# Kernel optimization log

Measured on AMD Instinct MI355X. Metric: run time of the kernel, lower is better.

Reference implementation:

```python
import jax, jax.numpy as jnp
import numpy as np

EPS = 1e-5
ABIT = 8
WBIT = 8


def ste_round(x):
    # straight-through rounding (HAWQ SymmetricQuantFunction)
    return x + jax.lax.stop_gradient(jnp.round(x) - x)


def quant_act(x, bit=ABIT):
    # per-tensor symmetric activation quantization (QuantAct)
    n = 2.0 ** (bit - 1) - 1  # 127
    scale = jnp.max(jnp.abs(x)) / n
    x_int = jnp.clip(ste_round(x / scale), -n - 1, n)
    return x_int * scale, scale


def setup_inputs() -> dict:
    key = jax.random.key(0)
    k = jax.random.split(key, 6)
    B, C_in, H, W, C_out = 32, 512, 32, 32, 128
    x = jax.random.normal(k[0], (B, C_in, H, W), jnp.float32)
    # incoming activation scale (input assumed already 8-bit quantized)
    act_scaling_factor = (jnp.max(jnp.abs(x)) / 127.0).reshape(1)
    bn_gamma = jax.random.uniform(k[1], (C_in,), jnp.float32, 0.5, 1.5)
    bn_beta = jax.random.normal(k[2], (C_in,), jnp.float32) * 0.1
    bn_mean = jax.random.normal(k[3], (C_in,), jnp.float32) * 0.1
    bn_var = jax.random.uniform(k[4], (C_in,), jnp.float32, 0.5, 1.5)
    conv_weight = jax.random.normal(k[5], (C_out, C_in, 3, 3), jnp.float32) / np.sqrt(C_in * 9)
    return {"x": x, "act_scaling_factor": act_scaling_factor,
            "bn_gamma": bn_gamma, "bn_beta": bn_beta,
            "bn_mean": bn_mean, "bn_var": bn_var,
            "conv_weight": conv_weight}


def reference(x, act_scaling_factor, bn_gamma, bn_beta, bn_mean, bn_var, conv_weight):
    nw = 2.0 ** (WBIT - 1) - 1  # 127
    s_in = act_scaling_factor.reshape(())

    # ---- QuantBn: fold BN into per-channel affine, quantize weight/bias ----
    w_bn = bn_gamma / jnp.sqrt(bn_var + EPS)            # [C_in]
    b_bn = bn_beta - bn_mean * w_bn                      # [C_in]
    ws_bn = jnp.max(jnp.abs(w_bn)) / nw                  # per-tensor weight scale
    w_int = jnp.clip(ste_round(w_bn / ws_bn), -nw - 1, nw)
    bn_sf = ws_bn * s_in                                 # bn output scaling factor
    b_int = ste_round(b_bn / bn_sf)
    x_int = x / s_in
    x = (x_int * w_int[None, :, None, None] + b_int[None, :, None, None]) * bn_sf

    # ---- ReLU ----
    x = jax.nn.relu(x)

    # ---- QuantAct: requantize activations to 8 bit ----
    x, s_act = quant_act(x)

    # ---- QuantConv2d: per-output-channel 8-bit weight quant, int conv ----
    ws_c = jnp.max(jnp.abs(conv_weight), axis=(1, 2, 3)) / nw       # [C_out]
    w_cint = jnp.clip(ste_round(conv_weight / ws_c[:, None, None, None]), -nw - 1, nw)
    y_int = jax.lax.conv_general_dilated(
        x / s_act, w_cint, window_strides=(1, 1), padding=((1, 1), (1, 1)),
        dimension_numbers=("NCHW", "OIHW", "NCHW"))
    conv_sf = s_act * ws_c                               # [C_out]
    y = y_int * conv_sf[None, :, None, None]

    # ---- QuantAct output requant ----
    y, s_out = quant_act(y)
    return (y, s_out)
```

## Files before the change

kernel.cpp:

```cpp
#include <hip/hip_runtime.h>


typedef int v4i __attribute__((ext_vector_type(4)));

#define WS_A1    64
#define WS_B1    2176
#define WS_WSC   4224
#define WS_WQ    8192
#define WS_X2    602112
#define WS_ZROW  18427904

__device__ __forceinline__ float wave_max(float m) {
#pragma unroll
    for (int off = 32; off; off >>= 1) m = fmaxf(m, __shfl_xor(m, off));
    return m;
}

__global__ __launch_bounds__(512) void k_prep(
    const float* __restrict__ gamma, const float* __restrict__ beta,
    const float* __restrict__ mean,  const float* __restrict__ var,
    const float* __restrict__ asf,   const float* __restrict__ cw,
    float* ws_f, unsigned* ws_u, float* __restrict__ wsc,
    signed char* __restrict__ wq) {
    int t = threadIdx.x;
    __shared__ float red[8];
    if (blockIdx.x == 128) {
        float wbn = gamma[t] / sqrtf(var[t] + 1e-5f);
        float bbn = beta[t] - mean[t] * wbn;
        float m = wave_max(fabsf(wbn));
        if ((t & 63) == 0) red[t >> 6] = m;
        __syncthreads();
        float mall = red[0];
#pragma unroll
        for (int i = 1; i < 8; ++i) mall = fmaxf(mall, red[i]);
        float ws_bn = mall / 127.0f;
        float s_in  = asf[0];
        float bn_sf = ws_bn * s_in;
        float wint  = fminf(fmaxf(rintf(wbn / ws_bn), -128.f), 127.f);
        float bint  = rintf(bbn / bn_sf);
        ws_f[WS_A1 / 4 + t] = wint * bn_sf / s_in;
        ws_f[WS_B1 / 4 + t] = bint * bn_sf;
        if (t == 0) { ws_u[0] = 0u; ws_u[1] = 0u; }
    } else {
        int co = blockIdx.x;
        const float* w = cw + (size_t)co * 4608;
        float m = 0.f;
        for (int j = t; j < 4608; j += 512) m = fmaxf(m, fabsf(w[j]));
        m = wave_max(m);
        if ((t & 63) == 0) red[t >> 6] = m;
        __syncthreads();
        float mall = red[0];
#pragma unroll
        for (int i = 1; i < 8; ++i) mall = fmaxf(mall, red[i]);
        float sc = mall / 127.0f;
        if (t == 0) wsc[co] = sc;
        for (int j = t; j < 4608; j += 512) {
            float q = fminf(fmaxf(rintf(w[j] / sc), -128.f), 127.f);
            int c = j / 9, tap = j - c * 9;
            wq[(((size_t)tap * 8 + (c >> 6)) * 128 + co) * 64 + (c & 63)] = (signed char)q;
        }
    }
}

__global__ __launch_bounds__(256) void k_xmax(
    const float4* __restrict__ x4, const float* __restrict__ ws_f,
    unsigned* __restrict__ amax) {
    const float* A1 = ws_f + WS_A1 / 4;
    const float* B1 = ws_f + WS_B1 / 4;
    float m = 0.f;
    int stride = gridDim.x * blockDim.x;
    for (int i = blockIdx.x * blockDim.x + threadIdx.x; i < 4194304; i += stride) {
        float4 v = x4[i];
        int c = (i >> 8) & 511;
        float A = A1[c], B = B1[c];
        m = fmaxf(m, fmaxf(fmaxf(fmaf(v.x, A, B), fmaf(v.y, A, B)),
                           fmaxf(fmaf(v.z, A, B), fmaf(v.w, A, B))));
    }
    __shared__ float red[4];
    m = wave_max(m);
    if ((threadIdx.x & 63) == 0) red[threadIdx.x >> 6] = m;
    __syncthreads();
    if (threadIdx.x == 0) {
        m = fmaxf(fmaxf(red[0], red[1]), fmaxf(red[2], red[3]));
        atomicMax(amax, __float_as_uint(m));
    }
}

__global__ __launch_bounds__(256) void k_xquant(
    const float4* __restrict__ x4, const float* __restrict__ ws_f,
    const unsigned* __restrict__ amax, unsigned* __restrict__ x2u,
    unsigned* __restrict__ zrowu) {
    int bb = blockIdx.x >> 5, h = blockIdx.x & 31;
    float inv_sact = 127.0f / __uint_as_float(amax[0]);
    const float* A1 = ws_f + WS_A1 / 4;
    const float* B1 = ws_f + WS_B1 / 4;
    int t = threadIdx.x;

    {
        int cc = t >> 5, rem = t & 31;
        int wp = (rem >> 4) * 33, inner = rem & 15;
        x2u[((size_t)(((bb * 32 + h) * 8 + cc) * 34 + wp)) * 16 + inner] = 0u;
    }
    if (blockIdx.x < 17) {
        int idx = blockIdx.x * 256 + t;
        if (idx < 4352) zrowu[idx] = 0u;
    }

    __shared__ unsigned lds[512 * 9];

#pragma unroll
    for (int it = 0; it < 16; ++it) {
        int idx = it * 256 + t;
        int c = idx >> 3, f4 = idx & 7;
        float4 v = x4[((size_t)bb * 512 + c) * 256 + h * 8 + f4];
        float A = A1[c] * inv_sact, B = B1[c] * inv_sact;
        unsigned q0 = (unsigned)(int)fminf(rintf(fmaxf(fmaf(v.x, A, B), 0.f)), 127.f);
        unsigned q1 = (unsigned)(int)fminf(rintf(fmaxf(fmaf(v.y, A, B), 0.f)), 127.f);
        unsigned q2 = (unsigned)(int)fminf(rintf(fmaxf(fmaf(v.z, A, B), 0.f)), 127.f);
        unsigned q3 = (unsigned)(int)fminf(rintf(fmaxf(fmaf(v.w, A, B), 0.f)), 127.f);
        lds[c * 9 + f4] = q0 | (q1 << 8) | (q2 << 16) | (q3 << 24);
    }
    __syncthreads();

#pragma unroll
    for (int it2 = 0; it2 < 4; ++it2) {
        int cdw = (t & 31) + ((t >> 6) << 5);
        int wq4 = ((t >> 5) & 1) + (it2 << 1);
        unsigned u0 = lds[(4 * cdw + 0) * 9 + wq4];
        unsigned u1 = lds[(4 * cdw + 1) * 9 + wq4];
        unsigned u2 = lds[(4 * cdw + 2) * 9 + wq4];
        unsigned u3 = lds[(4 * cdw + 3) * 9 + wq4];
        int cc = cdw >> 4, inner = cdw & 15;
        unsigned* dst = x2u + ((size_t)(((bb * 32 + h) * 8 + cc) * 34 + wq4 * 4 + 1)) * 16 + inner;
#pragma unroll
        for (int k = 0; k < 4; ++k) {
            unsigned o = ((u0 >> (8 * k)) & 255) | (((u1 >> (8 * k)) & 255) << 8) |
                         (((u2 >> (8 * k)) & 255) << 16) | (((u3 >> (8 * k)) & 255) << 24);
            dst[(size_t)k * 16] = o;
        }
    }
}

__global__ __launch_bounds__(256, 2) void k_conv(
    const unsigned char* __restrict__ x2, const unsigned char* __restrict__ zrow,
    const signed char* __restrict__ wq,
    const float* __restrict__ wsc, const unsigned* __restrict__ amax,
    unsigned* __restrict__ amaxy, float* __restrict__ y) {
    __shared__ v4i red[2][1024];
    int t = threadIdx.x;
    int lane = t & 63, kv = t >> 6;
    int m = lane & 15, quad = lane >> 4;

    int bid = blockIdx.x;
    int tile = (bid & 7) * 128 + (bid >> 3);
    int ch = tile & 1;
    int rowpair = (tile >> 1) & 15;
    int bb = tile >> 5;
    int h0 = rowpair * 2;
    int co0 = ch * 64;

    const unsigned char* xb = x2 + (size_t)bb * (32 * 8 * 34 * 64);
    const unsigned char* rp[4];
#pragma unroll
    for (int j = 0; j < 4; ++j) {
        int row = h0 - 1 + j;
        rp[j] = ((unsigned)row < 32u) ? (xb + (size_t)row * (8 * 34 * 64)) : zrow;
    }

    v4i acc[4][4];
#pragma unroll
    for (int i = 0; i < 4; ++i)
#pragma unroll
        for (int j = 0; j < 4; ++j) acc[i][j] = (v4i){0, 0, 0, 0};

    const v4i* pwv = (const v4i*)wq + (co0 + m) * 4 + quad;

#pragma unroll
    for (int kh = 0; kh < 3; ++kh)
#pragma unroll
        for (int kw = 0; kw < 3; ++kw) {
            int tap = kh * 3 + kw;
#pragma unroll
            for (int cc = 0; cc < 2; ++cc) {
                int ci = kv * 2 + cc;
                v4i a[4];
#pragma unroll
                for (int mt = 0; mt < 4; ++mt)
                    a[mt] = *((const v4i*)rp[kh + (mt >> 1)] +
                              (ci * 34 + m + (mt & 1) * 16 + kw) * 4 + quad);
#pragma unroll
                for (int nt = 0; nt < 4; ++nt) {
                    v4i bf = pwv[tap * 4096 + ci * 512 + nt * 64];
#pragma unroll
                    for (int mt = 0; mt < 4; ++mt)
                        acc[mt][nt] = __builtin_amdgcn_mfma_i32_16x16x64_i8(a[mt], bf, acc[mt][nt], 0, 0, 0);
                }
            }
        }

    if (kv >= 2) {
#pragma unroll
        for (int mt = 0; mt < 4; ++mt)
#pragma unroll
            for (int nt = 0; nt < 4; ++nt)
                red[kv - 2][(mt * 4 + nt) * 64 + lane] = acc[mt][nt];
    }
    __syncthreads();
    if (kv < 2) {
#pragma unroll
        for (int mt = 0; mt < 4; ++mt)
#pragma unroll
            for (int nt = 0; nt < 4; ++nt) {
                v4i p = red[kv][(mt * 4 + nt) * 64 + lane];
                acc[mt][nt].x += p.x; acc[mt][nt].y += p.y;
                acc[mt][nt].z += p.z; acc[mt][nt].w += p.w;
            }
    }
    __syncthreads();
    if (kv == 1) {
#pragma unroll
        for (int mt = 0; mt < 4; ++mt)
#pragma unroll
            for (int nt = 0; nt < 4; ++nt)
                red[0][(mt * 4 + nt) * 64 + lane] = acc[mt][nt];
    }
    __syncthreads();
    if (kv == 0) {
#pragma unroll
        for (int mt = 0; mt < 4; ++mt)
#pragma unroll
            for (int nt = 0; nt < 4; ++nt) {
                v4i p = red[0][(mt * 4 + nt) * 64 + lane];
                acc[mt][nt].x += p.x; acc[mt][nt].y += p.y;
                acc[mt][nt].z += p.z; acc[mt][nt].w += p.w;
            }

        float s_act = __uint_as_float(amax[0]) / 127.0f;
        float mx = 0.f;
#pragma unroll
        for (int nt = 0; nt < 4; ++nt) {
            int co = co0 + nt * 16 + m;
            float sf = s_act * wsc[co];
#pragma unroll
            for (int mt = 0; mt < 4; ++mt) {
                int row = h0 + (mt >> 1);
                float* yb = y + ((size_t)(bb * 128 + co)) * 1024 + row * 32 + (mt & 1) * 16;
                float4 vv;
                vv.x = (float)acc[mt][nt][0] * sf;
                vv.y = (float)acc[mt][nt][1] * sf;
                vv.z = (float)acc[mt][nt][2] * sf;
                vv.w = (float)acc[mt][nt][3] * sf;
                *(float4*)(yb + quad * 4) = vv;
                mx = fmaxf(mx, fmaxf(fmaxf(fabsf(vv.x), fabsf(vv.y)),
                                     fmaxf(fabsf(vv.z), fabsf(vv.w))));
            }
        }
        mx = wave_max(mx);
        if (lane == 0) atomicMax(amaxy, __float_as_uint(mx));
    }
}

__global__ __launch_bounds__(256) void k_yquant(float* __restrict__ yout,
                                                const unsigned* __restrict__ ws_u) {
    float s_out = __uint_as_float(ws_u[1]) / 127.0f;
    float4* y4 = (float4*)yout;
    int stride = gridDim.x * blockDim.x;
    for (int i = blockIdx.x * blockDim.x + threadIdx.x; i < 1048576; i += stride) {
        float4 v = y4[i];
        v.x = fminf(fmaxf(rintf(v.x / s_out), -128.f), 127.f) * s_out;
        v.y = fminf(fmaxf(rintf(v.y / s_out), -128.f), 127.f) * s_out;
        v.z = fminf(fmaxf(rintf(v.z / s_out), -128.f), 127.f) * s_out;
        v.w = fminf(fmaxf(rintf(v.w / s_out), -128.f), 127.f) * s_out;
        y4[i] = v;
    }
    if (blockIdx.x == 0 && threadIdx.x == 0) yout[4194304] = s_out;
}

extern "C" void kernel_launch(void* const* d_in, const int* in_sizes, int n_in,
                              void* d_out, int out_size, void* d_ws, size_t ws_size,
                              hipStream_t stream) {
    const float* x     = (const float*)d_in[0];
    const float* asf   = (const float*)d_in[1];
    const float* gamma = (const float*)d_in[2];
    const float* beta  = (const float*)d_in[3];
    const float* mean  = (const float*)d_in[4];
    const float* var   = (const float*)d_in[5];
    const float* cw    = (const float*)d_in[6];

    float*    ws_f = (float*)d_ws;
    unsigned* ws_u = (unsigned*)d_ws;
    signed char*   wq   = (signed char*)d_ws + WS_WQ;
    unsigned char* x2   = (unsigned char*)d_ws + WS_X2;
    unsigned char* zrow = (unsigned char*)d_ws + WS_ZROW;
    float* y = (float*)d_out;

    k_prep<<<129, 512, 0, stream>>>(gamma, beta, mean, var, asf, cw,
                                    ws_f, ws_u, ws_f + WS_WSC / 4, wq);
    k_xmax<<<1024, 256, 0, stream>>>((const float4*)x, ws_f, ws_u);
    k_xquant<<<1024, 256, 0, stream>>>((const float4*)x, ws_f, ws_u,
                                       (unsigned*)x2, (unsigned*)zrow);
    k_conv<<<1024, 256, 0, stream>>>(x2, zrow, wq, ws_f + WS_WSC / 4,
                                     ws_u, ws_u + 1, y);
    k_yquant<<<1024, 256, 0, stream>>>(y, ws_u);
}
```

Baseline: 184.7 us.

## Derive activation max from per-channel raw min/max, drop separate xmax pass

Replaces the atomic global max over the BN-affine-transformed input with per-channel min/max of raw x computed inside the prep kernel. Because the affine map is monotonic per channel, the post-BN max can be rebuilt from those extremes, and each xquant block recomputes it redundantly. This removes the atomic and the dependency on it. The prep kernel now also reads all of x, so the extra full pass is folded into a wider launch rather than eliminated. Separately, conv occupancy is raised to 3 and the cross-wave reduction is flattened into one LDS stage, which needs a larger shared buffer.

```diff
diff --git a/kernel.cpp b/kernel.cpp
--- a/kernel.cpp
+++ b/kernel.cpp
@@ -6,7 +6,9 @@
 #define WS_A1    64
 #define WS_B1    2176
 #define WS_WSC   4224
-#define WS_WQ    8192
+#define WS_XMX   4736
+#define WS_XMN   6784
+#define WS_WQ    12288
 #define WS_X2    602112
 #define WS_ZROW  18427904
 
@@ -20,11 +22,31 @@
     const float* __restrict__ gamma, const float* __restrict__ beta,
     const float* __restrict__ mean,  const float* __restrict__ var,
     const float* __restrict__ asf,   const float* __restrict__ cw,
+    const float4* __restrict__ x4,
     float* ws_f, unsigned* ws_u, float* __restrict__ wsc,
     signed char* __restrict__ wq) {
     int t = threadIdx.x;
-    __shared__ float red[8];
-    if (blockIdx.x == 128) {
+    int bid = blockIdx.x;
+    __shared__ float red[16];
+    if (bid < 128) {
+        int co = bid;
+        const float* w = cw + (size_t)co * 4608;
+        float m = 0.f;
+        for (int j = t; j < 4608; j += 512) m = fmaxf(m, fabsf(w[j]));
+        m = wave_max(m);
+        if ((t & 63) == 0) red[t >> 6] = m;
+        __syncthreads();
+        float mall = red[0];
+#pragma unroll
+        for (int i = 1; i < 8; ++i) mall = fmaxf(mall, red[i]);
+        float sc = mall / 127.0f;
+        if (t == 0) wsc[co] = sc;
+#pragma unroll
+        for (int tap = 0; tap < 9; ++tap) {
+            float q = fminf(fmaxf(rintf(w[t * 9 + tap] / sc), -128.f), 127.f);
+            wq[(((size_t)(tap * 8 + (t >> 6)) * 128 + co) * 64) + (t & 63)] = (signed char)q;
+        }
+    } else if (bid == 128) {
         float wbn = gamma[t] / sqrtf(var[t] + 1e-5f);
         float bbn = beta[t] - mean[t] * wbn;
         float m = wave_max(fabsf(wbn));
@@ -40,61 +62,55 @@
         float bint  = rintf(bbn / bn_sf);
         ws_f[WS_A1 / 4 + t] = wint * bn_sf / s_in;
         ws_f[WS_B1 / 4 + t] = bint * bn_sf;
-        if (t == 0) { ws_u[0] = 0u; ws_u[1] = 0u; }
+        if (t == 0) ws_u[1] = 0u;
     } else {
-        int co = blockIdx.x;
-        const float* w = cw + (size_t)co * 4608;
-        float m = 0.f;
-        for (int j = t; j < 4608; j += 512) m = fmaxf(m, fabsf(w[j]));
-        m = wave_max(m);
-        if ((t & 63) == 0) red[t >> 6] = m;
+        int c = bid - 129;
+        float mx = -3.4e38f, mn = 3.4e38f;
+#pragma unroll
+        for (int r = 0; r < 16; ++r) {
+            int bbb = r * 2 + (t >> 8);
+            float4 v = x4[((size_t)(bbb * 512 + c)) * 256 + (t & 255)];
+            mx = fmaxf(mx, fmaxf(fmaxf(v.x, v.y), fmaxf(v.z, v.w)));
+            mn = fminf(mn, fminf(fminf(v.x, v.y), fminf(v.z, v.w)));
+        }
+        mx = wave_max(mx);
+        mn = -wave_max(-mn);
+        if ((t & 63) == 0) { red[t >> 6] = mx; red[8 + (t >> 6)] = mn; }
         __syncthreads();
-        float mall = red[0];
-#pragma unroll
-        for (int i = 1; i < 8; ++i) mall = fmaxf(mall, red[i]);
-        float sc = mall / 127.0f;
-        if (t == 0) wsc[co] = sc;
-        for (int j = t; j < 4608; j += 512) {
-            float q = fminf(fmaxf(rintf(w[j] / sc), -128.f), 127.f);
-            int c = j / 9, tap = j - c * 9;
-            wq[(((size_t)tap * 8 + (c >> 6)) * 128 + co) * 64 + (c & 63)] = (signed char)q;
-        }
-    }
-}
-
-__global__ __launch_bounds__(256) void k_xmax(
-    const float4* __restrict__ x4, const float* __restrict__ ws_f,
-    unsigned* __restrict__ amax) {
+        if (t == 0) {
+            float M = red[0], N = red[8];
+#pragma unroll
+            for (int i = 1; i < 8; ++i) { M = fmaxf(M, red[i]); N = fminf(N, red[8 + i]); }
+            ws_f[WS_XMX / 4 + c] = M;
+            ws_f[WS_XMN / 4 + c] = N;
+        }
+    }
+}
+
+__global__ __launch_bounds__(256) void k_xquant(
+    const float4* __restrict__ x4, float* __restrict__ ws_f,
+    unsigned* __restrict__ x2u, unsigned* __restrict__ zrowu) {
+    int bb = blockIdx.x >> 5, h = blockIdx.x & 31;
     const float* A1 = ws_f + WS_A1 / 4;
     const float* B1 = ws_f + WS_B1 / 4;
-    float m = 0.f;
-    int stride = gridDim.x * blockDim.x;
-    for (int i = blockIdx.x * blockDim.x + threadIdx.x; i < 4194304; i += stride) {
-        float4 v = x4[i];
-        int c = (i >> 8) & 511;
+    const float* XMX = ws_f + WS_XMX / 4;
+    const float* XMN = ws_f + WS_XMN / 4;
+    int t = threadIdx.x;
+
+    __shared__ float sred[4];
+    float cand = 0.f;
+#pragma unroll
+    for (int c0 = 0; c0 < 512; c0 += 256) {
+        int c = c0 + t;
         float A = A1[c], B = B1[c];
-        m = fmaxf(m, fmaxf(fmaxf(fmaf(v.x, A, B), fmaf(v.y, A, B)),
-                           fmaxf(fmaf(v.z, A, B), fmaf(v.w, A, B))));
-    }
-    __shared__ float red[4];
-    m = wave_max(m);
-    if ((threadIdx.x & 63) == 0) red[threadIdx.x >> 6] = m;
+        cand = fmaxf(cand, fmaxf(fmaf(XMX[c], A, B), fmaf(XMN[c], A, B)));
+    }
+    cand = wave_max(cand);
+    if ((t & 63) == 0) sred[t >> 6] = cand;
     __syncthreads();
-    if (threadIdx.x == 0) {
-        m = fmaxf(fmaxf(red[0], red[1]), fmaxf(red[2], red[3]));
-        atomicMax(amax, __float_as_uint(m));
-    }
-}
-
-__global__ __launch_bounds__(256) void k_xquant(
-    const float4* __restrict__ x4, const float* __restrict__ ws_f,
-    const unsigned* __restrict__ amax, unsigned* __restrict__ x2u,
-    unsigned* __restrict__ zrowu) {
-    int bb = blockIdx.x >> 5, h = blockIdx.x & 31;
-    float inv_sact = 127.0f / __uint_as_float(amax[0]);
-    const float* A1 = ws_f + WS_A1 / 4;
-    const float* B1 = ws_f + WS_B1 / 4;
-    int t = threadIdx.x;
+    float xm = fmaxf(fmaxf(sred[0], sred[1]), fmaxf(sred[2], sred[3]));
+    float inv_sact = 127.0f / xm;
+    if (blockIdx.x == 0 && t == 0) ws_f[3] = xm / 127.0f;
 
     {
         int cc = t >> 5, rem = t & 31;
@@ -141,12 +157,12 @@
     }
 }
 
-__global__ __launch_bounds__(256, 2) void k_conv(
+__global__ __launch_bounds__(256, 3) void k_conv(
     const unsigned char* __restrict__ x2, const unsigned char* __restrict__ zrow,
     const signed char* __restrict__ wq,
-    const float* __restrict__ wsc, const unsigned* __restrict__ amax,
+    const float* __restrict__ wsc, const float* __restrict__ ws_f,
     unsigned* __restrict__ amaxy, float* __restrict__ y) {
-    __shared__ v4i red[2][1024];
+    __shared__ v4i red[3][1024];
     int t = threadIdx.x;
     int lane = t & 63, kv = t >> 6;
     int m = lane & 15, quad = lane >> 4;
@@ -198,44 +214,27 @@
             }
         }
 
-    if (kv >= 2) {
+    if (kv > 0) {
 #pragma unroll
         for (int mt = 0; mt < 4; ++mt)
 #pragma unroll
             for (int nt = 0; nt < 4; ++nt)
-                red[kv - 2][(mt * 4 + nt) * 64 + lane] = acc[mt][nt];
-    }
-    __syncthreads();
-    if (kv < 2) {
-#pragma unroll
-        for (int mt = 0; mt < 4; ++mt)
-#pragma unroll
-            for (int nt = 0; nt < 4; ++nt) {
-                v4i p = red[kv][(mt * 4 + nt) * 64 + lane];
-                acc[mt][nt].x += p.x; acc[mt][nt].y += p.y;
-                acc[mt][nt].z += p.z; acc[mt][nt].w += p.w;
-            }
-    }
-    __syncthreads();
-    if (kv == 1) {
-#pragma unroll
-        for (int mt = 0; mt < 4; ++mt)
-#pragma unroll
-            for (int nt = 0; nt < 4; ++nt)
-                red[0][(mt * 4 + nt) * 64 + lane] = acc[mt][nt];
+                red[kv - 1][(mt * 4 + nt) * 64 + lane] = acc[mt][nt];
     }
     __syncthreads();
     if (kv == 0) {
 #pragma unroll
-        for (int mt = 0; mt < 4; ++mt)
-#pragma unroll
-            for (int nt = 0; nt < 4; ++nt) {
-                v4i p = red[0][(mt * 4 + nt) * 64 + lane];
-                acc[mt][nt].x += p.x; acc[mt][nt].y += p.y;
-                acc[mt][nt].z += p.z; acc[mt][nt].w += p.w;
-            }
-
-        float s_act = __uint_as_float(amax[0]) / 127.0f;
+        for (int r = 0; r < 3; ++r)
+#pragma unroll
+            for (int mt = 0; mt < 4; ++mt)
+#pragma unroll
+                for (int nt = 0; nt < 4; ++nt) {
+                    v4i p = red[r][(mt * 4 + nt) * 64 + lane];
+                    acc[mt][nt].x += p.x; acc[mt][nt].y += p.y;
+                    acc[mt][nt].z += p.z; acc[mt][nt].w += p.w;
+                }
+
+        float s_act = ws_f[3];
         float mx = 0.f;
 #pragma unroll
         for (int nt = 0; nt < 4; ++nt) {
@@ -294,12 +293,12 @@
     unsigned char* zrow = (unsigned char*)d_ws + WS_ZROW;
     float* y = (float*)d_out;
 
-    k_prep<<<129, 512, 0, stream>>>(gamma, beta, mean, var, asf, cw,
-                                    ws_f, ws_u, ws_f + WS_WSC / 4, wq);
-    k_xmax<<<1024, 256, 0, stream>>>((const float4*)x, ws_f, ws_u);
-    k_xquant<<<1024, 256, 0, stream>>>((const float4*)x, ws_f, ws_u,
+    k_prep<<<641, 512, 0, stream>>>(gamma, beta, mean, var, asf, cw,
+                                    (const float4*)x, ws_f, ws_u,
+                                    ws_f + WS_WSC / 4, wq);
+    k_xquant<<<1024, 256, 0, stream>>>((const float4*)x, ws_f,
                                        (unsigned*)x2, (unsigned*)zrow);
     k_conv<<<1024, 256, 0, stream>>>(x2, zrow, wq, ws_f + WS_WSC / 4,
-                                     ws_u, ws_u + 1, y);
+                                     ws_f, ws_u + 1, y);
     k_yquant<<<1024, 256, 0, stream>>>(y, ws_u);
 }
```

Result: faster. 176.5 us (-4.5%).
